# Kernel tuning notes

Hardware: AMD Instinct MI355X
Metric: run time of the kernel (lower is better)

Reference implementation:

```python
import jax, jax.numpy as jnp
import numpy as np

EPS = 1e-4  # ReEig clamp


def _spectral(X, f):
    # eigendecompose symmetric X and apply f to eigenvalues: V diag(f(w)) V^T
    w, v = jnp.linalg.eigh(X)
    return jnp.einsum('...ij,...j,...kj->...ik', v, f(w), v)


def _bimap(W, X):
    # W @ X @ W.T with W [out,in], X [b,in,in]
    return jnp.einsum('ij,bjk,lk->bil', W, X, W)


def setup_inputs() -> dict:
    key = jax.random.key(0)
    k1, k2, k3, k4 = jax.random.split(key, 4)
    B = 262144
    vech = jax.random.normal(k1, (B, 6), dtype=jnp.float32)
    # Stiefel init: Q factor of a Gaussian (orthonormal columns)
    W1 = jnp.linalg.qr(jax.random.normal(k2, (5, 3), dtype=jnp.float32))[0]
    W2 = jnp.linalg.qr(jax.random.normal(k3, (7, 5), dtype=jnp.float32))[0]
    W3 = jnp.linalg.qr(jax.random.normal(k4, (9, 7), dtype=jnp.float32))[0]
    return {"vech": vech, "W1": W1, "W2": W2, "W3": W3}


def reference(vech, W1, W2, W3):
    k = 3
    B = vech.shape[0]
    iu = jnp.triu_indices(k)
    X = jnp.zeros((B, k, k), dtype=vech.dtype).at[:, iu[0], iu[1]].set(vech)
    d = jnp.diagonal(X, axis1=-2, axis2=-1)  # [B,3]
    X = X + jnp.swapaxes(X, -2, -1) - d[..., :, None] * jnp.eye(k, dtype=vech.dtype)
    # SPDNet chain
    X = _spectral(X, jnp.exp)                      # ExpEig -> [B,3,3]
    X = _bimap(W1, X)                              # [B,5,5]
    X = _spectral(X, lambda w: jnp.maximum(w, EPS))  # ReEig
    X = _bimap(W2, X)                              # [B,7,7]
    X = _spectral(X, lambda w: jnp.maximum(w, EPS))
    X = _bimap(W3, X)                              # [B,9,9]
    X = _spectral(X, lambda w: jnp.maximum(w, EPS))
    return X
```

## Files before the change

### kernel.cpp

```cpp
#include <hip/hip_runtime.h>

#define EPSV 1e-4f

__device__ __forceinline__ void jrot(float& app, float& aqq, float& apq,
                                     float& arp, float& arq,
                                     float& vap, float& vaq,
                                     float& vbp, float& vbq,
                                     float& vcp, float& vcq) {
  const float apq0 = apq;
  float tau = (aqq - app) / (2.0f * apq0);
  float t = copysignf(1.0f / (fabsf(tau) + sqrtf(fmaf(tau, tau, 1.0f))), tau);
  if (apq0 == 0.0f) t = 0.0f;
  const float c = rsqrtf(fmaf(t, t, 1.0f));
  const float s = t * c;
  const float d = t * apq0;
  app -= d; aqq += d; apq = 0.0f;
  const float rp = arp, rq = arq;
  arp = c * rp - s * rq;
  arq = s * rp + c * rq;
  float x, y;
  x = vap; y = vaq; vap = c * x - s * y; vaq = s * x + c * y;
  x = vbp; y = vbq; vbp = c * x - s * y; vbq = s * x + c * y;
  x = vcp; y = vcq; vcp = c * x - s * y; vcq = s * x + c * y;
}

__global__ __launch_bounds__(256, 2) void spd_decoder_kernel(
    const float* __restrict__ vech, const float* __restrict__ W1,
    const float* __restrict__ W2, const float* __restrict__ W3,
    float* __restrict__ out, int B) {
  __shared__ float Tsh[21];
  __shared__ float Msh[27];
  __shared__ __align__(16) float buf[4][2592];

  const int tid = threadIdx.x;

  if (tid < 21) {
    const int r = tid / 3, c = tid % 3;
    float acc = 0.f;
#pragma unroll
    for (int j = 0; j < 5; ++j) acc += W2[r * 5 + j] * W1[j * 3 + c];
    Tsh[tid] = acc;
  }
  __syncthreads();
  if (tid < 27) {
    const int r = tid / 3, c = tid % 3;
    float acc = 0.f;
#pragma unroll
    for (int j = 0; j < 7; ++j) acc += W3[r * 7 + j] * Tsh[j * 3 + c];
    Msh[tid] = acc;
  }
  __syncthreads();

  const int e = blockIdx.x * 256 + tid;
  const float2* vp = reinterpret_cast<const float2*>(vech + (size_t)e * 6);
  const float2 p0 = vp[0], p1 = vp[1], p2 = vp[2];
  float a00 = p0.x, a01 = p0.y, a02 = p1.x, a11 = p1.y, a12 = p2.x, a22 = p2.y;

  float v00 = 1.f, v01 = 0.f, v02 = 0.f;
  float v10 = 0.f, v11 = 1.f, v12 = 0.f;
  float v20 = 0.f, v21 = 0.f, v22 = 1.f;
#pragma unroll
  for (int sweep = 0; sweep < 5; ++sweep) {
    jrot(a00, a11, a01, a02, a12, v00, v01, v10, v11, v20, v21);
    jrot(a00, a22, a02, a01, a12, v00, v02, v10, v12, v20, v22);
    jrot(a11, a22, a12, a01, a02, v01, v02, v11, v12, v21, v22);
  }

  const float e0 = expf(a00) - EPSV;
  const float e1 = expf(a11) - EPSV;
  const float e2 = expf(a22) - EPSV;

  float g0[9], g1[9], g2[9];
#pragma unroll
  for (int i = 0; i < 9; ++i) {
    const float m0 = Msh[i * 3 + 0], m1 = Msh[i * 3 + 1], m2 = Msh[i * 3 + 2];
    g0[i] = fmaf(m0, v00, fmaf(m1, v10, m2 * v20));
    g1[i] = fmaf(m0, v01, fmaf(m1, v11, m2 * v21));
    g2[i] = fmaf(m0, v02, fmaf(m1, v12, m2 * v22));
  }

  const int w = tid >> 6, l = tid & 63;
  float* wbuf = &buf[w][0];
  const size_t base = (size_t)(blockIdx.x * 256 + w * 64) * 81;

#pragma unroll
  for (int h = 0; h < 2; ++h) {
    if ((l >> 5) == h) {
      const int ll = l & 31;
      float* dst = wbuf + ll * 81;
#pragma unroll
      for (int i = 0; i < 9; ++i) {
        const float t0 = e0 * g0[i], t1 = e1 * g1[i], t2 = e2 * g2[i];
#pragma unroll
        for (int j = 0; j < 9; ++j) {
          float val = fmaf(t0, g0[j], fmaf(t1, g1[j], t2 * g2[j]));
          if (i == j) val += EPSV;
          dst[i * 9 + j] = val;
        }
      }
    }
    asm volatile("s_waitcnt lgkmcnt(0)" ::: "memory");
    __builtin_amdgcn_sched_barrier(0);

    const size_t sb = base + (size_t)h * 2592;
    const float4* rbuf = reinterpret_cast<const float4*>(wbuf);
    float4* outv = reinterpret_cast<float4*>(out + sb);
#pragma unroll
    for (int it = 0; it < 10; ++it) outv[it * 64 + l] = rbuf[it * 64 + l];
    if (l < 8) outv[640 + l] = rbuf[640 + l];

    asm volatile("s_waitcnt lgkmcnt(0)" ::: "memory");
    __builtin_amdgcn_sched_barrier(0);
  }
}

extern "C" void kernel_launch(void* const* d_in, const int* in_sizes, int n_in,
                              void* d_out, int out_size, void* d_ws, size_t ws_size,
                              hipStream_t stream) {
  const float* vech = (const float*)d_in[0];
  const float* W1 = (const float*)d_in[1];
  const float* W2 = (const float*)d_in[2];
  const float* W3 = (const float*)d_in[3];
  float* out = (float*)d_out;
  const int B = in_sizes[0] / 6;
  dim3 grid(B / 256), block(256);
  hipLaunchKernelGGL(spd_decoder_kernel, grid, block, 0, stream,
                     vech, W1, W2, W3, out, B);
}
```

Baseline: 24.31 us.

## Split each 9x9 output matrix across two lanes to remove divergent halves

Each matrix is now handled by a lane pair instead of one thread. Both lanes recompute the 3x3 Jacobi eigendecomposition, and each writes about half the columns of the 9x9 outer product into LDS. This removes the earlier two-pass scheme where half the wavefront sat idle while the other half wrote, and it halves the per-thread store work. The cost is duplicated eigen work per matrix and twice as many blocks.

```diff
diff --git a/kernel.cpp b/kernel.cpp
--- a/kernel.cpp
+++ b/kernel.cpp
@@ -51,7 +51,11 @@
   }
   __syncthreads();
 
-  const int e = blockIdx.x * 256 + tid;
+  const int w = tid >> 6, l = tid & 63;
+  const int q = l & 31;
+  const int hi = l >> 5;
+
+  const int e = blockIdx.x * 128 + w * 32 + q;
   const float2* vp = reinterpret_cast<const float2*>(vech + (size_t)e * 6);
   const float2 p0 = vp[0], p1 = vp[1], p2 = vp[2];
   float a00 = p0.x, a01 = p0.y, a02 = p1.x, a11 = p1.y, a12 = p2.x, a22 = p2.y;
@@ -79,39 +83,43 @@
     g2[i] = fmaf(m0, v02, fmaf(m1, v12, m2 * v22));
   }
 
-  const int w = tid >> 6, l = tid & 63;
-  float* wbuf = &buf[w][0];
-  const size_t base = (size_t)(blockIdx.x * 256 + w * 64) * 81;
+  float h0[5], h1[5], h2[5];
+#pragma unroll
+  for (int jl = 0; jl < 4; ++jl) {
+    h0[jl] = hi ? g0[jl + 5] : g0[jl];
+    h1[jl] = hi ? g1[jl + 5] : g1[jl];
+    h2[jl] = hi ? g2[jl + 5] : g2[jl];
+  }
+  h0[4] = g0[4]; h1[4] = g1[4]; h2[4] = g2[4];
+  const float epslo = hi ? 0.f : EPSV;
+  const float epshi = hi ? EPSV : 0.f;
 
+  float* dst = &buf[w][q * 81 + hi * 5];
 #pragma unroll
-  for (int h = 0; h < 2; ++h) {
-    if ((l >> 5) == h) {
-      const int ll = l & 31;
-      float* dst = wbuf + ll * 81;
+  for (int i = 0; i < 9; ++i) {
+    const float t0 = e0 * g0[i], t1 = e1 * g1[i], t2 = e2 * g2[i];
 #pragma unroll
-      for (int i = 0; i < 9; ++i) {
-        const float t0 = e0 * g0[i], t1 = e1 * g1[i], t2 = e2 * g2[i];
-#pragma unroll
-        for (int j = 0; j < 9; ++j) {
-          float val = fmaf(t0, g0[j], fmaf(t1, g1[j], t2 * g2[j]));
-          if (i == j) val += EPSV;
-          dst[i * 9 + j] = val;
-        }
+    for (int jl = 0; jl < 5; ++jl) {
+      float val = fmaf(t0, h0[jl], fmaf(t1, h1[jl], t2 * h2[jl]));
+      if (i == jl) val += epslo;
+      if (i == jl + 5) val += epshi;
+      if (jl < 4) {
+        dst[i * 9 + jl] = val;
+      } else if (!hi) {
+        dst[i * 9 + 4] = val;
       }
     }
-    asm volatile("s_waitcnt lgkmcnt(0)" ::: "memory");
-    __builtin_amdgcn_sched_barrier(0);
+  }
 
-    const size_t sb = base + (size_t)h * 2592;
-    const float4* rbuf = reinterpret_cast<const float4*>(wbuf);
-    float4* outv = reinterpret_cast<float4*>(out + sb);
+  asm volatile("s_waitcnt lgkmcnt(0)" ::: "memory");
+  __builtin_amdgcn_sched_barrier(0);
+
+  const size_t eb = (size_t)(blockIdx.x * 128 + w * 32) * 81;
+  const float4* rbuf = reinterpret_cast<const float4*>(&buf[w][0]);
+  float4* outv = reinterpret_cast<float4*>(out + eb);
 #pragma unroll
-    for (int it = 0; it < 10; ++it) outv[it * 64 + l] = rbuf[it * 64 + l];
-    if (l < 8) outv[640 + l] = rbuf[640 + l];
-
-    asm volatile("s_waitcnt lgkmcnt(0)" ::: "memory");
-    __builtin_amdgcn_sched_barrier(0);
-  }
+  for (int it = 0; it < 10; ++it) outv[it * 64 + l] = rbuf[it * 64 + l];
+  if (l < 8) outv[640 + l] = rbuf[640 + l];
 }
 
 extern "C" void kernel_launch(void* const* d_in, const int* in_sizes, int n_in,
@@ -123,7 +131,7 @@
   const float* W3 = (const float*)d_in[3];
   float* out = (float*)d_out;
   const int B = in_sizes[0] / 6;
-  dim3 grid(B / 256), block(256);
+  dim3 grid(B / 128), block(256);
   hipLaunchKernelGGL(spd_decoder_kernel, grid, block, 0, stream,
                      vech, W1, W2, W3, out, B);
 }
```

New measurement: 30.22 us. 24.3% more time.
